# Optimization experiments

Measured on AMD Instinct MI355X. Metric: run time of the kernel, lower is better.

The kernel has to match this reference:

```python
import jax, jax.numpy as jnp
import numpy as np

DIM = 1024
HEADS = 16
HEAD_DIM = DIM // HEADS
B, N = 4, 4096


def setup_inputs() -> dict:
    key = jax.random.key(0)
    k1, k2, k3, k4, k5 = jax.random.split(key, 5)
    scale_in = 1.0 / np.sqrt(DIM)
    return {
        "x": jax.random.normal(k1, (B, N, DIM), dtype=jnp.float32),
        # torch nn.Linear convention: weight [out, in], y = x @ W.T + b
        "w_qkv": jax.random.uniform(k2, (3 * DIM, DIM), jnp.float32, -scale_in, scale_in),
        "b_qkv": jax.random.uniform(k3, (3 * DIM,), jnp.float32, -scale_in, scale_in),
        "w_proj": jax.random.uniform(k4, (DIM, DIM), jnp.float32, -scale_in, scale_in),
        "b_proj": jax.random.uniform(k5, (DIM,), jnp.float32, -scale_in, scale_in),
    }


def reference(x, w_qkv, b_qkv, w_proj, b_proj):
    Bx, Nx, C = x.shape
    H, D = HEADS, HEAD_DIM
    qkv = (x @ w_qkv.T + b_qkv).reshape(Bx, Nx, 3, H, D)
    q, k, v = qkv[:, :, 0], qkv[:, :, 1], qkv[:, :, 2]  # each [B, N, H, D]
    # NOTE: faithful to source — heads dim was NOT moved to batch position,
    # so attention mixes across heads per token: scores [B, N, H, H].
    scores = jnp.einsum('bnhd,bngd->bnhg', q, k) / jnp.sqrt(jnp.asarray(D, x.dtype))
    attn = jax.nn.softmax(scores, axis=-1)
    out = jnp.einsum('bnhg,bngd->bnhd', attn, v).reshape(Bx, Nx, C)
    return out @ w_proj.T + b_proj
```

## Files before the change

kernel.cpp:

```cpp
#include <hip/hip_runtime.h>
#include <hip/hip_bf16.h>
#include <stdint.h>

typedef __bf16 v8bf __attribute__((ext_vector_type(8)));
typedef float  v4f  __attribute__((ext_vector_type(4)));
typedef unsigned short u16;

#define NTOK 16384
#define KDIM 1024

__device__ __forceinline__ u16 f2bf(float f) {
  uint32_t b = __builtin_bit_cast(uint32_t, f);
  b += 0x7FFFu + ((b >> 16) & 1u);
  return (u16)(b >> 16);
}

__device__ __forceinline__ void gl_lds16(const u16* g, u16* l) {
  __builtin_amdgcn_global_load_lds(
      (const __attribute__((address_space(1))) uint32_t*)g,
      (__attribute__((address_space(3))) uint32_t*)l,
      16, 0, 0);
}

__device__ __forceinline__ void bar() {
  __builtin_amdgcn_sched_barrier(0);
  __builtin_amdgcn_s_barrier();
  __builtin_amdgcn_sched_barrier(0);
}
#define LGKM0() do { asm volatile("s_waitcnt lgkmcnt(0)" ::: "memory"); \
                     __builtin_amdgcn_sched_barrier(0); } while (0)
#define VMW(n)  do { asm volatile("s_waitcnt vmcnt(" #n ")" ::: "memory"); \
                     __builtin_amdgcn_sched_barrier(0); } while (0)

__global__ void cvt_all(const float* __restrict__ x, const float* __restrict__ wq,
                        const float* __restrict__ wp, u16* __restrict__ xo,
                        u16* __restrict__ wqo, u16* __restrict__ wpo) {
  size_t id = (size_t)blockIdx.x * 256 + threadIdx.x;
  const float* src; u16* dst;
  if (id < 2097152)      { src = x  + id * 8;              dst = xo  + id * 8; }
  else if (id < 2490368) { src = wq + (id - 2097152) * 8;  dst = wqo + (id - 2097152) * 8; }
  else                   { src = wp + (id - 2490368) * 8;  dst = wpo + (id - 2490368) * 8; }
  float4 a = *(const float4*)(src);
  float4 b = *(const float4*)(src + 4);
  union { u16 u[8]; uint4 v; } pk;
  pk.u[0]=f2bf(a.x); pk.u[1]=f2bf(a.y); pk.u[2]=f2bf(a.z); pk.u[3]=f2bf(a.w);
  pk.u[4]=f2bf(b.x); pk.u[5]=f2bf(b.y); pk.u[6]=f2bf(b.z); pk.u[7]=f2bf(b.w);
  *(uint4*)(dst) = pk.v;
}

template<int NTOT, bool OUT_BF16>
__global__ __launch_bounds__(512, 2)
void gemm_bt(const u16* __restrict__ A, const u16* __restrict__ Bw,
             const float* __restrict__ bias, void* __restrict__ out) {
  constexpr int NM = NTOK / 256;
  constexpr int NN = NTOT / 256;
  constexpr int NWG = NM * NN;
  constexpr int NT = KDIM / 32;
  const int bid = blockIdx.x;
  const int swz = (bid & 7) * (NWG / 8) + (bid >> 3);
  const int bm = swz % NM, bn = swz / NM;

  __shared__ __align__(16) u16 lds[2][2][256 * 32];

  const int tid = threadIdx.x, lane = tid & 63, w = tid >> 6;
  const int wr = w >> 2, wc = w & 3;

  v4f acc[8][4];
#pragma unroll
  for (int i = 0; i < 8; ++i)
#pragma unroll
    for (int j = 0; j < 4; ++j) acc[i][j] = v4f{0.f, 0.f, 0.f, 0.f};

  const u16* Ab = A  + (size_t)bm * 256 * KDIM;
  const u16* Bb = Bw + (size_t)bn * 256 * KDIM;

  const size_t soff0 = (size_t)(tid >> 2) * KDIM
      + (size_t)((((tid & 3) ^ ((tid >> 2) & 3) ^ ((tid >> 4) & 3)) & 3) * 8);
  auto stage2 = [&](u16* dst, const u16* src) {
    gl_lds16(src + soff0, dst + (size_t)tid * 8);
    gl_lds16(src + soff0 + (size_t)128 * KDIM, dst + (size_t)tid * 8 + 4096);
  };

  const int cks = ((lane >> 4) ^ (lane & 3) ^ ((lane >> 2) & 3)) & 3;
  const int aoff = (wr * 128 + (lane & 15)) * 32 + cks * 8;
  const int boff = (wc * 64  + (lane & 15)) * 32 + cks * 8;

#define HALFSTEP(CUR, TA, TB) do {                                            \
  const u16* La_ = lds[CUR][0];                                               \
  const u16* Lb_ = lds[CUR][1];                                               \
  v8bf af[4], bf4[4];                                                         \
  _Pragma("unroll") for (int f = 0; f < 4; ++f)                               \
    af[f] = *(const v8bf*)(La_ + aoff + f * 512);                             \
  _Pragma("unroll") for (int f = 0; f < 4; ++f)                               \
    bf4[f] = *(const v8bf*)(Lb_ + boff + f * 512);                            \
  if ((TA) < NT) stage2(&lds[(CUR) ^ 1][0][0], Ab + (size_t)(TA) * 32);       \
  bar(); LGKM0();                                                             \
  __builtin_amdgcn_s_setprio(1);                                              \
  _Pragma("unroll") for (int qi = 0; qi < 4; ++qi)                            \
  _Pragma("unroll") for (int qj = 0; qj < 4; ++qj)                            \
    acc[qi][qj] = __builtin_amdgcn_mfma_f32_16x16x32_bf16(                    \
        af[qi], bf4[qj], acc[qi][qj], 0, 0, 0);                               \
  __builtin_amdgcn_s_setprio(0);                                              \
  bar();                                                                      \
  _Pragma("unroll") for (int f = 0; f < 4; ++f)                               \
    af[f] = *(const v8bf*)(La_ + aoff + (f + 4) * 512);                       \
  if ((TB) < NT) stage2(&lds[CUR][1][0], Bb + (size_t)(TB) * 32);             \
  bar(); LGKM0();                                                             \
  __builtin_amdgcn_s_setprio(1);                                              \
  _Pragma("unroll") for (int qi = 0; qi < 4; ++qi)                            \
  _Pragma("unroll") for (int qj = 0; qj < 4; ++qj)                            \
    acc[4 + qi][qj] = __builtin_amdgcn_mfma_f32_16x16x32_bf16(                \
        af[qi], bf4[qj], acc[4 + qi][qj], 0, 0, 0);                           \
  __builtin_amdgcn_s_setprio(0);                                              \
  if ((TB) < NT) { VMW(2); } else { VMW(0); }                                 \
  bar();                                                                      \
} while (0)

  stage2(&lds[0][1][0], Bb);
  stage2(&lds[0][0][0], Ab);
  stage2(&lds[1][1][0], Bb + 32);
  VMW(2);
  bar();

  for (int j = 0; j < NT / 2; ++j) {
    HALFSTEP(0, 2 * j + 1, 2 * j + 2);
    HALFSTEP(1, 2 * j + 2, 2 * j + 3);
  }
#undef HALFSTEP

  const int col0 = bn * 256 + wc * 64 + (lane & 15);
  const int row0 = bm * 256 + wr * 128 + ((lane >> 4) << 2);
#pragma unroll
  for (int mf = 0; mf < 8; ++mf) {
#pragma unroll
    for (int nf = 0; nf < 4; ++nf) {
      const int gc = col0 + nf * 16;
      const float bv = bias[gc];
#pragma unroll
      for (int j = 0; j < 4; ++j) {
        const size_t idx = (size_t)(row0 + mf * 16 + j) * NTOT + gc;
        const float v = acc[mf][nf][j] + bv;
        if constexpr (OUT_BF16) ((u16*)out)[idx] = f2bf(v);
        else                    ((float*)out)[idx] = v;
      }
    }
  }
}

__global__ __launch_bounds__(256)
void attn_mix(const u16* __restrict__ qkv, u16* __restrict__ outp) {
  __shared__ __align__(16) u16 sq[4][3072];
  __shared__ float sp[4][16][16];
  const int tid = threadIdx.x, lane = tid & 63, w = tid >> 6;
  const size_t tok = (size_t)blockIdx.x * 4 + w;
  const u16* src = qkv + tok * 3072;
#pragma unroll
  for (int i = 0; i < 6; ++i) {
    int t = i * 64 + lane;
    int row = t >> 3;
    int c = (t & 7) ^ (row & 7);
    gl_lds16(src + row * 64 + c * 8, &sq[w][t * 8]);
  }
  __syncthreads();

  const int h = lane >> 2, gb = lane & 3;
  v8bf qv[8];
#pragma unroll
  for (int c = 0; c < 8; ++c)
    qv[c] = *(const v8bf*)&sq[w][h * 64 + ((c ^ (h & 7)) * 8)];

  float s[4];
#pragma unroll
  for (int g4 = 0; g4 < 4; ++g4) {
    const int g = gb * 4 + g4;
    float a = 0.f;
#pragma unroll
    for (int c = 0; c < 8; ++c) {
      v8bf kv = *(const v8bf*)&sq[w][1024 + g * 64 + ((c ^ (g & 7)) * 8)];
#pragma unroll
      for (int j = 0; j < 8; ++j) a += (float)qv[c][j] * (float)kv[j];
    }
    s[g4] = a * 0.125f;
  }
  float m = fmaxf(fmaxf(s[0], s[1]), fmaxf(s[2], s[3]));
  m = fmaxf(m, __shfl_xor(m, 1));
  m = fmaxf(m, __shfl_xor(m, 2));
  float p[4], sum = 0.f;
#pragma unroll
  for (int g4 = 0; g4 < 4; ++g4) { p[g4] = __expf(s[g4] - m); sum += p[g4]; }
  sum += __shfl_xor(sum, 1);
  sum += __shfl_xor(sum, 2);
  const float inv = 1.f / sum;
#pragma unroll
  for (int g4 = 0; g4 < 4; ++g4) sp[w][h][gb * 4 + g4] = p[g4] * inv;
  __syncthreads();

  float o[16];
#pragma unroll
  for (int j = 0; j < 16; ++j) o[j] = 0.f;
  const int db = gb;
#pragma unroll
  for (int g = 0; g < 16; ++g) {
    const float a = sp[w][h][g];
    v8bf v0 = *(const v8bf*)&sq[w][2048 + g * 64 + (((db * 2)     ^ (g & 7)) * 8)];
    v8bf v1 = *(const v8bf*)&sq[w][2048 + g * 64 + (((db * 2 + 1) ^ (g & 7)) * 8)];
#pragma unroll
    for (int j = 0; j < 8; ++j) { o[j] += a * (float)v0[j]; o[8 + j] += a * (float)v1[j]; }
  }
  union { u16 u[16]; uint4 v[2]; } ob;
#pragma unroll
  for (int j = 0; j < 16; ++j) ob.u[j] = f2bf(o[j]);
  u16* dst = outp + tok * 1024 + h * 64 + db * 16;
  *(uint4*)dst = ob.v[0];
  *((uint4*)dst + 1) = ob.v[1];
}

extern "C" void kernel_launch(void* const* d_in, const int* in_sizes, int n_in,
                              void* d_out, int out_size, void* d_ws, size_t ws_size,
                              hipStream_t stream) {
  const float* x      = (const float*)d_in[0];
  const float* w_qkv  = (const float*)d_in[1];
  const float* b_qkv  = (const float*)d_in[2];
  const float* w_proj = (const float*)d_in[3];
  const float* b_proj = (const float*)d_in[4];

  char* ws = (char*)d_ws;
  u16* x_bf    = (u16*)(ws);
  u16* wqkv_bf = (u16*)(ws + (size_t)33554432);
  u16* wp_bf   = (u16*)(ws + (size_t)39845888);
  u16* qkv_bf  = (u16*)(ws + (size_t)41943040);
  u16* at_bf   = (u16*)(ws + (size_t)142606336);

  cvt_all<<<dim3(10240), dim3(256), 0, stream>>>(x, w_qkv, w_proj,
                                                 x_bf, wqkv_bf, wp_bf);

  gemm_bt<3072, true ><<<dim3(768), dim3(512), 0, stream>>>(x_bf, wqkv_bf, b_qkv, qkv_bf);
  attn_mix<<<dim3(4096), dim3(256), 0, stream>>>(qkv_bf, at_bf);
  gemm_bt<1024, false><<<dim3(256), dim3(512), 0, stream>>>(at_bf, wp_bf, b_proj, d_out);
}
```

Measured before the change: 221.9 us.

## Deepen GEMM LDS pipeline to four stages with dynamic shared memory

Replaces the two-buffer half-step A/B staging with a four-stage ring buffer in 128 KiB of dynamic LDS. Three tiles are prefetched ahead and the vmcnt waits are relaxed, so more global loads stay in flight to hide memory latency. Launch bounds drop to one workgroup per CU because of the larger LDS footprint. That halves occupancy and adds a per-launch hipFuncSetAttribute call.

```diff
diff --git a/kernel.cpp b/kernel.cpp
--- a/kernel.cpp
+++ b/kernel.cpp
@@ -49,7 +49,7 @@
 }
 
 template<int NTOT, bool OUT_BF16>
-__global__ __launch_bounds__(512, 2)
+__global__ __launch_bounds__(512, 1)
 void gemm_bt(const u16* __restrict__ A, const u16* __restrict__ Bw,
              const float* __restrict__ bias, void* __restrict__ out) {
   constexpr int NM = NTOK / 256;
@@ -60,7 +60,9 @@
   const int swz = (bid & 7) * (NWG / 8) + (bid >> 3);
   const int bm = swz % NM, bn = swz / NM;
 
-  __shared__ __align__(16) u16 lds[2][2][256 * 32];
+  extern __shared__ __align__(16) u16 smem[];
+  u16* ldsA = smem;
+  u16* ldsB = smem + 4 * 8192;
 
   const int tid = threadIdx.x, lane = tid & 63, w = tid >> 6;
   const int wr = w >> 2, wc = w & 3;
@@ -76,7 +78,7 @@
 
   const size_t soff0 = (size_t)(tid >> 2) * KDIM
       + (size_t)((((tid & 3) ^ ((tid >> 2) & 3) ^ ((tid >> 4) & 3)) & 3) * 8);
-  auto stage2 = [&](u16* dst, const u16* src) {
+  auto stageT = [&](u16* dst, const u16* src) {
     gl_lds16(src + soff0, dst + (size_t)tid * 8);
     gl_lds16(src + soff0 + (size_t)128 * KDIM, dst + (size_t)tid * 8 + 4096);
   };
@@ -85,15 +87,16 @@
   const int aoff = (wr * 128 + (lane & 15)) * 32 + cks * 8;
   const int boff = (wc * 64  + (lane & 15)) * 32 + cks * 8;
 
-#define HALFSTEP(CUR, TA, TB) do {                                            \
-  const u16* La_ = lds[CUR][0];                                               \
-  const u16* Lb_ = lds[CUR][1];                                               \
+#define TILE(ST, U, DO_STAGE, VMODE) do {                                     \
+  const u16* La_ = ldsA + (ST) * 8192;                                        \
+  const u16* Lb_ = ldsB + (ST) * 8192;                                        \
   v8bf af[4], bf4[4];                                                         \
   _Pragma("unroll") for (int f = 0; f < 4; ++f)                               \
     af[f] = *(const v8bf*)(La_ + aoff + f * 512);                             \
   _Pragma("unroll") for (int f = 0; f < 4; ++f)                               \
     bf4[f] = *(const v8bf*)(Lb_ + boff + f * 512);                            \
-  if ((TA) < NT) stage2(&lds[(CUR) ^ 1][0][0], Ab + (size_t)(TA) * 32);       \
+  if (DO_STAGE) stageT(ldsA + (((ST) + 3) & 3) * 8192,                        \
+                       Ab + (size_t)(U) * 32);                                \
   bar(); LGKM0();                                                             \
   __builtin_amdgcn_s_setprio(1);                                              \
   _Pragma("unroll") for (int qi = 0; qi < 4; ++qi)                            \
@@ -104,7 +107,8 @@
   bar();                                                                      \
   _Pragma("unroll") for (int f = 0; f < 4; ++f)                               \
     af[f] = *(const v8bf*)(La_ + aoff + (f + 4) * 512);                       \
-  if ((TB) < NT) stage2(&lds[CUR][1][0], Bb + (size_t)(TB) * 32);             \
+  if (DO_STAGE) stageT(ldsB + (((ST) + 3) & 3) * 8192,                        \
+                       Bb + (size_t)(U) * 32);                                \
   bar(); LGKM0();                                                             \
   __builtin_amdgcn_s_setprio(1);                                              \
   _Pragma("unroll") for (int qi = 0; qi < 4; ++qi)                            \
@@ -112,21 +116,30 @@
     acc[4 + qi][qj] = __builtin_amdgcn_mfma_f32_16x16x32_bf16(                \
         af[qi], bf4[qj], acc[4 + qi][qj], 0, 0, 0);                           \
   __builtin_amdgcn_s_setprio(0);                                              \
-  if ((TB) < NT) { VMW(2); } else { VMW(0); }                                 \
+  if ((VMODE) == 0) { VMW(8); }                                               \
+  else if ((VMODE) == 1) { VMW(4); }                                          \
+  else if ((VMODE) == 2) { VMW(0); }                                          \
   bar();                                                                      \
 } while (0)
 
-  stage2(&lds[0][1][0], Bb);
-  stage2(&lds[0][0][0], Ab);
-  stage2(&lds[1][1][0], Bb + 32);
-  VMW(2);
+  stageT(ldsA + 0,     Ab);        stageT(ldsB + 0,     Bb);
+  stageT(ldsA + 8192,  Ab + 32);   stageT(ldsB + 8192,  Bb + 32);
+  stageT(ldsA + 16384, Ab + 64);   stageT(ldsB + 16384, Bb + 64);
+  VMW(8);
   bar();
 
-  for (int j = 0; j < NT / 2; ++j) {
-    HALFSTEP(0, 2 * j + 1, 2 * j + 2);
-    HALFSTEP(1, 2 * j + 2, 2 * j + 3);
-  }
-#undef HALFSTEP
+  for (int j = 0; j < 7; ++j) {
+    const int t0 = 4 * j;
+    TILE(0, t0 + 3, 1, 0);
+    TILE(1, t0 + 4, 1, 0);
+    TILE(2, t0 + 5, 1, 0);
+    TILE(3, t0 + 6, 1, 0);
+  }
+  TILE(0, 31, 1, 0);
+  TILE(1, 0, 0, 1);
+  TILE(2, 0, 0, 2);
+  TILE(3, 0, 0, 3);
+#undef TILE
 
   const int col0 = bn * 256 + wc * 64 + (lane & 15);
   const int row0 = bm * 256 + wr * 128 + ((lane >> 4) << 2);
@@ -231,10 +244,15 @@
   u16* qkv_bf  = (u16*)(ws + (size_t)41943040);
   u16* at_bf   = (u16*)(ws + (size_t)142606336);
 
+  (void)hipFuncSetAttribute((const void*)&gemm_bt<3072, true>,
+                            hipFuncAttributeMaxDynamicSharedMemorySize, 131072);
+  (void)hipFuncSetAttribute((const void*)&gemm_bt<1024, false>,
+                            hipFuncAttributeMaxDynamicSharedMemorySize, 131072);
+
   cvt_all<<<dim3(10240), dim3(256), 0, stream>>>(x, w_qkv, w_proj,
                                                  x_bf, wqkv_bf, wp_bf);
 
-  gemm_bt<3072, true ><<<dim3(768), dim3(512), 0, stream>>>(x_bf, wqkv_bf, b_qkv, qkv_bf);
+  gemm_bt<3072, true ><<<dim3(768), dim3(512), 131072, stream>>>(x_bf, wqkv_bf, b_qkv, qkv_bf);
   attn_mix<<<dim3(4096), dim3(256), 0, stream>>>(qkv_bf, at_bf);
-  gemm_bt<1024, false><<<dim3(256), dim3(512), 0, stream>>>(at_bf, wp_bf, b_proj, d_out);
-}
+  gemm_bt<1024, false><<<dim3(256), dim3(512), 131072, stream>>>(at_bf, wp_bf, b_proj, d_out);
+}
```

Result: slower. 228.1 us (+2.8%).

## Deepen GEMM K-tile to 64 with dynamic LDS and split-half staging schedule

Applied to the files above, without the earlier changes.

Doubles the K depth per pipeline stage from 32 to 64, halving the number of barrier-separated iterations. LDS moves to 128 KB of dynamic shared memory holding two full 256x64 A/B buffers, with an 8-way XOR swizzle in place of the old 4-way one. Each tile is split into four MFMA quarters, and the next tile's quarter-slabs are staged between them. The aim is less sync and issue overhead per MFMA, at the cost of twice the LDS per workgroup, which likely limits occupancy to one block per CU despite launch_bounds(512,2).

```diff
diff --git a/kernel.cpp b/kernel.cpp
--- a/kernel.cpp
+++ b/kernel.cpp
@@ -55,12 +55,12 @@
   constexpr int NM = NTOK / 256;
   constexpr int NN = NTOT / 256;
   constexpr int NWG = NM * NN;
-  constexpr int NT = KDIM / 32;
+  constexpr int NT = KDIM / 64;
   const int bid = blockIdx.x;
   const int swz = (bid & 7) * (NWG / 8) + (bid >> 3);
   const int bm = swz % NM, bn = swz / NM;
 
-  __shared__ __align__(16) u16 lds[2][2][256 * 32];
+  extern __shared__ __align__(16) u16 smem[];
 
   const int tid = threadIdx.x, lane = tid & 63, w = tid >> 6;
   const int wr = w >> 2, wc = w & 3;
@@ -74,59 +74,86 @@
   const u16* Ab = A  + (size_t)bm * 256 * KDIM;
   const u16* Bb = Bw + (size_t)bn * 256 * KDIM;
 
-  const size_t soff0 = (size_t)(tid >> 2) * KDIM
-      + (size_t)((((tid & 3) ^ ((tid >> 2) & 3) ^ ((tid >> 4) & 3)) & 3) * 8);
-  auto stage2 = [&](u16* dst, const u16* src) {
-    gl_lds16(src + soff0, dst + (size_t)tid * 8);
-    gl_lds16(src + soff0 + (size_t)128 * KDIM, dst + (size_t)tid * 8 + 4096);
+  const int srow = tid >> 3;
+  const int sc   = (tid & 7) ^ (srow & 7);
+  const size_t soff = (size_t)srow * KDIM + (size_t)sc * 8;
+  auto stageH = [&](int dstoff, const u16* src) {
+    gl_lds16(src + soff, smem + dstoff + (size_t)tid * 8);
+    gl_lds16(src + soff + (size_t)64 * KDIM, smem + dstoff + (size_t)tid * 8 + 4096);
   };
 
-  const int cks = ((lane >> 4) ^ (lane & 3) ^ ((lane >> 2) & 3)) & 3;
-  const int aoff = (wr * 128 + (lane & 15)) * 32 + cks * 8;
-  const int boff = (wc * 64  + (lane & 15)) * 32 + cks * 8;
-
-#define HALFSTEP(CUR, TA, TB) do {                                            \
-  const u16* La_ = lds[CUR][0];                                               \
-  const u16* Lb_ = lds[CUR][1];                                               \
-  v8bf af[4], bf4[4];                                                         \
+  const int rA  = lane & 15;
+  const int ck0 = (((lane >> 4) ^ (lane & 7)) << 3);
+  const int ck1 = ((((lane >> 4) + 4) ^ (lane & 7)) << 3);
+  const int ha = wr * 8192;
+  const int hb = 16384 + (wc >> 1) * 8192 + (wc & 1) * 64 * 64;
+
+  v8bf Af[4][2], B0[2][2], B1[2][2];
+
+#define MM16(FI, GI, BF) do {                                                 \
   _Pragma("unroll") for (int f = 0; f < 4; ++f)                               \
-    af[f] = *(const v8bf*)(La_ + aoff + f * 512);                             \
-  _Pragma("unroll") for (int f = 0; f < 4; ++f)                               \
-    bf4[f] = *(const v8bf*)(Lb_ + boff + f * 512);                            \
-  if ((TA) < NT) stage2(&lds[(CUR) ^ 1][0][0], Ab + (size_t)(TA) * 32);       \
+  _Pragma("unroll") for (int g = 0; g < 2; ++g) {                             \
+    acc[(FI)+f][(GI)+g] = __builtin_amdgcn_mfma_f32_16x16x32_bf16(            \
+        Af[f][0], BF[g][0], acc[(FI)+f][(GI)+g], 0, 0, 0);                    \
+    acc[(FI)+f][(GI)+g] = __builtin_amdgcn_mfma_f32_16x16x32_bf16(            \
+        Af[f][1], BF[g][1], acc[(FI)+f][(GI)+g], 0, 0, 0);                    \
+  }                                                                           \
+} while (0)
+
+#define TILE(T, D, DN, ST, VM) do {                                           \
+                                                            \
+  _Pragma("unroll") for (int f = 0; f < 4; ++f) {                             \
+    Af[f][0] = *(const v8bf*)(smem + (D) + ha + (f*16 + rA)*64 + ck0);        \
+    Af[f][1] = *(const v8bf*)(smem + (D) + ha + (f*16 + rA)*64 + ck1); }      \
+  _Pragma("unroll") for (int g = 0; g < 2; ++g) {                             \
+    B0[g][0] = *(const v8bf*)(smem + (D) + hb + (g*16 + rA)*64 + ck0);        \
+    B0[g][1] = *(const v8bf*)(smem + (D) + hb + (g*16 + rA)*64 + ck1); }      \
+  if (ST) stageH((DN) + 8192, Ab + (size_t)128*KDIM + (size_t)((T)+1)*64);    \
   bar(); LGKM0();                                                             \
-  __builtin_amdgcn_s_setprio(1);                                              \
-  _Pragma("unroll") for (int qi = 0; qi < 4; ++qi)                            \
-  _Pragma("unroll") for (int qj = 0; qj < 4; ++qj)                            \
-    acc[qi][qj] = __builtin_amdgcn_mfma_f32_16x16x32_bf16(                    \
-        af[qi], bf4[qj], acc[qi][qj], 0, 0, 0);                               \
+  __builtin_amdgcn_s_setprio(1); MM16(0, 0, B0);                              \
+  __builtin_amdgcn_s_setprio(0); bar();                                       \
+                                                            \
+  _Pragma("unroll") for (int g = 0; g < 2; ++g) {                             \
+    B1[g][0] = *(const v8bf*)(smem + (D) + hb + (32 + g*16 + rA)*64 + ck0);   \
+    B1[g][1] = *(const v8bf*)(smem + (D) + hb + (32 + g*16 + rA)*64 + ck1); } \
+  if (ST) stageH((DN) + 16384, Bb + (size_t)((T)+1)*64);                      \
+  bar(); LGKM0();                                                             \
+  __builtin_amdgcn_s_setprio(1); MM16(0, 2, B1);                              \
+  __builtin_amdgcn_s_setprio(0); bar();                                       \
+                                                            \
+  _Pragma("unroll") for (int f = 0; f < 4; ++f) {                             \
+    Af[f][0] = *(const v8bf*)(smem + (D) + ha + (64 + f*16 + rA)*64 + ck0);   \
+    Af[f][1] = *(const v8bf*)(smem + (D) + ha + (64 + f*16 + rA)*64 + ck1); } \
+  if (ST) stageH((DN) + 24576, Bb + (size_t)128*KDIM + (size_t)((T)+1)*64);   \
+  bar(); LGKM0();                                                             \
+  __builtin_amdgcn_s_setprio(1); MM16(4, 2, B1);                              \
+  __builtin_amdgcn_s_setprio(0); bar();                                       \
+                                                            \
+  if ((VM) == 2) stageH((D) + 0, Ab + (size_t)((T)+2)*64);                    \
+  bar();                                                                      \
+  __builtin_amdgcn_s_setprio(1); MM16(4, 0, B0);                              \
   __builtin_amdgcn_s_setprio(0);                                              \
-  bar();                                                                      \
-  _Pragma("unroll") for (int f = 0; f < 4; ++f)                               \
-    af[f] = *(const v8bf*)(La_ + aoff + (f + 4) * 512);                       \
-  if ((TB) < NT) stage2(&lds[CUR][1][0], Bb + (size_t)(TB) * 32);             \
-  bar(); LGKM0();                                                             \
-  __builtin_amdgcn_s_setprio(1);                                              \
-  _Pragma("unroll") for (int qi = 0; qi < 4; ++qi)                            \
-  _Pragma("unroll") for (int qj = 0; qj < 4; ++qj)                            \
-    acc[4 + qi][qj] = __builtin_amdgcn_mfma_f32_16x16x32_bf16(                \
-        af[qi], bf4[qj], acc[4 + qi][qj], 0, 0, 0);                           \
-  __builtin_amdgcn_s_setprio(0);                                              \
-  if ((TB) < NT) { VMW(2); } else { VMW(0); }                                 \
+  if ((VM) == 2) { VMW(2); } else if ((VM) == 0) { VMW(0); }                  \
   bar();                                                                      \
 } while (0)
 
-  stage2(&lds[0][1][0], Bb);
-  stage2(&lds[0][0][0], Ab);
-  stage2(&lds[1][1][0], Bb + 32);
+  stageH(0,     Ab);
+  stageH(8192,  Ab + (size_t)128 * KDIM);
+  stageH(16384, Bb);
+  stageH(24576, Bb + (size_t)128 * KDIM);
+  stageH(32768, Ab + 64);
   VMW(2);
   bar();
 
-  for (int j = 0; j < NT / 2; ++j) {
-    HALFSTEP(0, 2 * j + 1, 2 * j + 2);
-    HALFSTEP(1, 2 * j + 2, 2 * j + 3);
-  }
-#undef HALFSTEP
+  for (int j = 0; j < 7; ++j) {
+    const int t0 = 2 * j;
+    TILE(t0,     0,     32768, 1, 2);
+    TILE(t0 + 1, 32768, 0,     1, 2);
+  }
+  TILE(14, 0,     32768, 1, 0);
+  TILE(15, 32768, 0,     0, -1);
+#undef TILE
+#undef MM16
 
   const int col0 = bn * 256 + wc * 64 + (lane & 15);
   const int row0 = bm * 256 + wr * 128 + ((lane >> 4) << 2);
@@ -231,10 +258,15 @@
   u16* qkv_bf  = (u16*)(ws + (size_t)41943040);
   u16* at_bf   = (u16*)(ws + (size_t)142606336);
 
+  (void)hipFuncSetAttribute((const void*)&gemm_bt<3072, true>,
+                            hipFuncAttributeMaxDynamicSharedMemorySize, 131072);
+  (void)hipFuncSetAttribute((const void*)&gemm_bt<1024, false>,
+                            hipFuncAttributeMaxDynamicSharedMemorySize, 131072);
+
   cvt_all<<<dim3(10240), dim3(256), 0, stream>>>(x, w_qkv, w_proj,
                                                  x_bf, wqkv_bf, wp_bf);
 
-  gemm_bt<3072, true ><<<dim3(768), dim3(512), 0, stream>>>(x_bf, wqkv_bf, b_qkv, qkv_bf);
+  gemm_bt<3072, true ><<<dim3(768), dim3(512), 131072, stream>>>(x_bf, wqkv_bf, b_qkv, qkv_bf);
   attn_mix<<<dim3(4096), dim3(256), 0, stream>>>(qkv_bf, at_bf);
-  gemm_bt<1024, false><<<dim3(256), dim3(512), 0, stream>>>(at_bf, wp_bf, b_proj, d_out);
-}
+  gemm_bt<1024, false><<<dim3(256), dim3(512), 131072, stream>>>(at_bf, wp_bf, b_proj, d_out);
+}
```

Measured after the change: 216.4 us. -2.5%, faster.
